# Optimization experiments

Hardware: AMD Instinct MI355X
Metric: run time of the kernel (lower is better)

## Reference

```python
import jax, jax.numpy as jnp
import numpy as np

B, L = 8, 2048
Q_IN, V_IN, QK, VD = 512, 1024, 96, 96


def _conv1d_same(x_bcl, w_oik, b_o):
    # x: (B, C, L), w: (O, I, K), 'same' padding, stride 1
    y = jax.lax.conv_general_dilated(
        x_bcl, w_oik, window_strides=(1,), padding='SAME',
        dimension_numbers=('NCH', 'OIH', 'NCH'))
    return y + b_o[None, :, None]


def masked_softmax(scores, seqlengths):
    # scores: (B, L, L); mask key positions >= seqlengths[b]
    mask = jnp.arange(scores.shape[-1])[None, None, :] < seqlengths[:, None, None]
    scores = jnp.where(mask, scores, jnp.float32(-1e6))
    return jax.nn.softmax(scores, axis=-1)


def setup_inputs() -> dict:
    key = jax.random.key(0)
    ks = jax.random.split(key, 12)
    def lin(k, fan_in, shape):
        bound = 1.0 / np.sqrt(fan_in)
        return jax.random.uniform(k, shape, jnp.float32, -bound, bound)
    return {
        'plm_embedding': jax.random.normal(ks[0], (B, L, V_IN), jnp.float32),
        'evo_local': jax.random.normal(ks[1], (B, L, Q_IN), jnp.float32),
        'seqlengths': jax.random.randint(ks[2], (B,), 1, L + 1),
        'q_w': lin(ks[3], Q_IN, (QK, Q_IN)), 'q_b': lin(ks[4], Q_IN, (QK,)),
        'k_w': lin(ks[5], Q_IN + 2 * VD, (QK, Q_IN + 2 * VD)), 'k_b': lin(ks[6], Q_IN + 2 * VD, (QK,)),
        'v_w': lin(ks[7], V_IN, (VD, V_IN)), 'v_b': lin(ks[8], V_IN, (VD,)),
        'cn3_w': lin(ks[9], Q_IN * 3, (QK, Q_IN, 3)), 'cn3_b': lin(ks[9], Q_IN * 3, (QK,)),
        'cn5_w': lin(ks[10], Q_IN * 5, (QK, Q_IN, 5)), 'cn5_b': lin(ks[11], Q_IN * 5, (QK,)),
    }


def reference(plm_embedding, evo_local, seqlengths, q_w, q_b, k_w, k_b, v_w, v_b,
              cn3_w, cn3_b, cn5_w, cn5_b):
    norm = jnp.float32(1.0 / np.sqrt(QK))
    Q = jnp.einsum('bld,od->blo', evo_local, q_w) + q_b          # (B,L,QK)
    x_bcl = jnp.transpose(evo_local, (0, 2, 1))                  # (B,C,L)
    k3 = _conv1d_same(x_bcl, cn3_w, cn3_b)                       # (B,QK,L)
    k5 = _conv1d_same(x_bcl, cn5_w, cn5_b)
    cat = jnp.concatenate(
        (evo_local, jnp.transpose(k3, (0, 2, 1)), jnp.transpose(k5, (0, 2, 1))), axis=2)
    K = jnp.einsum('bld,od->blo', cat, k_w) + k_b                # (B,L,QK)
    V = jnp.einsum('bld,od->blo', plm_embedding, v_w) + v_b      # (B,L,VD)
    scores = jnp.einsum('bqd,bkd->bqk', Q, K) * norm             # (B,L,L)
    atten = masked_softmax(scores, seqlengths)
    out = jnp.einsum('bqk,bkd->bqd', atten, V)
    return out + V
```

## Files before the change

kernel.cpp:

```cpp
#include <hip/hip_runtime.h>

typedef unsigned short u16;
typedef unsigned int u32;
typedef float f32x4 __attribute__((ext_vector_type(4)));
typedef short s16x8 __attribute__((ext_vector_type(8)));

#define LSEQ 2048
#define QIN 512
#define VIN 1024
#define KCAT 704
#define KEFF 2560
#define NORMS 0.10206207261596575f

__device__ __forceinline__ u16 f2bf(float f) {
  u32 u = __float_as_uint(f);
  u = (u + 0x7fffu + ((u >> 16) & 1u)) >> 16;
  return (u16)u;
}
__device__ __forceinline__ float bf2f(u16 v) {
  return __uint_as_float(((u32)v) << 16);
}

__device__ __forceinline__ s16x8 load8cvt(const float* __restrict__ p) {
  float4 a = *(const float4*)p;
  float4 b = *(const float4*)(p + 4);
  s16x8 r;
  r[0] = (short)f2bf(a.x); r[1] = (short)f2bf(a.y);
  r[2] = (short)f2bf(a.z); r[3] = (short)f2bf(a.w);
  r[4] = (short)f2bf(b.x); r[5] = (short)f2bf(b.y);
  r[6] = (short)f2bf(b.z); r[7] = (short)f2bf(b.w);
  return r;
}

__device__ __forceinline__ s16x8 cvt2x4(float4 a, float4 b) {
  s16x8 r;
  r[0] = (short)f2bf(a.x); r[1] = (short)f2bf(a.y);
  r[2] = (short)f2bf(a.z); r[3] = (short)f2bf(a.w);
  r[4] = (short)f2bf(b.x); r[5] = (short)f2bf(b.y);
  r[6] = (short)f2bf(b.z); r[7] = (short)f2bf(b.w);
  return r;
}

__device__ __forceinline__ size_t wfrag_idx(int o, int k) {
  int kc = k >> 5, kg = (k >> 3) & 3, j = k & 7;
  int nt = o >> 4, ln = o & 15;
  return ((size_t)(kc * 6 + nt) * 64 + kg * 16 + ln) * 8 + j;
}

__global__ __launch_bounds__(256) void prep1(
    const float* __restrict__ q_w, const float* __restrict__ k_w,
    const float* __restrict__ k_b, const float* __restrict__ v_w,
    const float* __restrict__ cn3_w, const float* __restrict__ cn3_b,
    const float* __restrict__ cn5_w, const float* __restrict__ cn5_b,
    float* __restrict__ c3t, float* __restrict__ c5t,
    u16* __restrict__ qwf, u16* __restrict__ vwf,
    u16* __restrict__ kw3f, u16* __restrict__ kw5f,
    float* __restrict__ beff) {
  int blk = blockIdx.x, tid = threadIdx.x;
  if (blk < 576) {
    int idx = blk * 256 + tid;
    int t = idx / (512 * 96);
    int rem = idx - t * 512 * 96;
    int c = rem / 96, j = rem - c * 96;
    c3t[idx] = cn3_w[(j * 512 + c) * 3 + t];
  } else if (blk < 1536) {
    int idx = (blk - 576) * 256 + tid;
    int t = idx / (512 * 96);
    int rem = idx - t * 512 * 96;
    int c = rem / 96, j = rem - c * 96;
    c5t[idx] = cn5_w[(j * 512 + c) * 5 + t];
  } else if (blk < 1728) {
    int e = (blk - 1536) * 256 + tid;
    int o = e >> 9, k = e & 511;
    qwf[wfrag_idx(o, k)] = f2bf(q_w[e]);
  } else if (blk < 2112) {
    int e = (blk - 1728) * 256 + tid;
    int o = e >> 10, k = e & 1023;
    vwf[wfrag_idx(o, k)] = f2bf(v_w[e]);
  } else if (blk < 2184) {
    int e = (blk - 2112) * 256 + tid;
    int half = e / 9216;
    int i = e - half * 9216;
    int o = i / 96, j = i - o * 96;
    float v = k_w[o * KCAT + (half ? 608 : 512) + j];
    size_t di = ((size_t)((j >> 5) * 6 + (o >> 4)) * 64 +
                 ((j >> 3) & 3) * 16 + (o & 15)) * 8 + (j & 7);
    (half ? kw5f : kw3f)[di] = f2bf(v);
  } else {
    if (tid < 96) {
      const float* kwo = k_w + tid * KCAT;
      float b = k_b[tid];
      for (int j = 0; j < 96; ++j)
        b += kwo[512 + j] * cn3_b[j] + kwo[608 + j] * cn5_b[j];
      beff[tid] = b;
    }
  }
}

__global__ __launch_bounds__(256) void prep2(
    const float* __restrict__ c3t, const float* __restrict__ c5t,
    const u16* __restrict__ kw3f, const u16* __restrict__ kw5f,
    const float* __restrict__ k_w, u16* __restrict__ wefff) {
  __shared__ float Ls[4][16][100];
  int blk = blockIdx.x, tid = threadIdx.x;
  int wid = tid >> 6, lane = tid & 63, ln = lane & 15, kg = lane >> 4;
  int k = blk * 64 + wid * 16 + ln;
  bool c3ok = (k >= 512) && (k < 2048);
  const float* a5 = c5t + (size_t)k * 96;
  const float* a3 = c3t + (size_t)(c3ok ? k - 512 : 0) * 96;
  f32x4 acc[6];
  #pragma unroll
  for (int nt = 0; nt < 6; ++nt) acc[nt] = (f32x4){0.f, 0.f, 0.f, 0.f};
  #pragma unroll
  for (int jc = 0; jc < 3; ++jc) {
    s16x8 aa5 = load8cvt(a5 + jc * 32 + kg * 8);
    s16x8 aa3 = (s16x8){0, 0, 0, 0, 0, 0, 0, 0};
    if (c3ok) aa3 = load8cvt(a3 + jc * 32 + kg * 8);
    const u16* b5 = kw5f + (size_t)jc * 3072 + lane * 8;
    const u16* b3 = kw3f + (size_t)jc * 3072 + lane * 8;
    #pragma unroll
    for (int nt = 0; nt < 6; ++nt) {
      acc[nt] = __builtin_amdgcn_mfma_f32_16x16x32_bf16(
          aa5, *(const s16x8*)&b5[nt * 512], acc[nt], 0, 0, 0);
      acc[nt] = __builtin_amdgcn_mfma_f32_16x16x32_bf16(
          aa3, *(const s16x8*)&b3[nt * 512], acc[nt], 0, 0, 0);
    }
  }
  #pragma unroll
  for (int nt = 0; nt < 6; ++nt)
    #pragma unroll
    for (int r = 0; r < 4; ++r)
      Ls[wid][kg * 4 + r][nt * 16 + ln] = acc[nt][r];
  asm volatile("s_waitcnt lgkmcnt(0)" ::: "memory");
  #pragma unroll
  for (int sl = 0; sl < 3; ++sl) {
    int slot = sl * 64 + lane;
    int o = slot >> 1, rc = slot & 1;
    int k0 = blk * 64 + wid * 16 + rc * 8;
    int t = k0 >> 9, cbase = k0 & 511;
    s16x8 ov;
    #pragma unroll
    for (int e = 0; e < 8; ++e) {
      float v = Ls[wid][rc * 8 + e][o];
      if (t == 2) v += k_w[o * KCAT + cbase + e];
      ov[e] = (short)f2bf(v);
    }
    *(s16x8*)&wefff[((size_t)((k0 >> 5) * 6 + (o >> 4)) * 64 +
                     ((k0 >> 3) & 3) * 16 + (o & 15)) * 8] = ov;
  }
}

__global__ __launch_bounds__(256, 2) void proj_fused(
    const float* __restrict__ evo, const float* __restrict__ plm,
    const u16* __restrict__ qwf, const u16* __restrict__ vwf,
    const u16* __restrict__ wefff, const float* __restrict__ q_b,
    const float* __restrict__ beff, const float* __restrict__ v_b,
    u16* __restrict__ Qf, u16* __restrict__ Kf,
    u16* __restrict__ Vfr, u16* __restrict__ Vb) {
  __shared__ u16 At[2 * 68 * 72];
  __shared__ u16 LBS[18432];
  float* Ls = (float*)LBS;
  int bxr = blockIdx.x, bb = blockIdx.y;
  int tid = threadIdx.x;
  int wid = tid >> 6, lane = tid & 63, ln = lane & 15, kg = lane >> 4;
  int srow = tid >> 2, spart = tid & 3;

  if (bxr < 32) {
    int bx = bxr;
    int r0 = bx * 64;
    const float* xb = evo + (size_t)bb * LSEQ * QIN;
    bool halo = tid < 16;
    int hrow = 64 + (tid >> 2);

    float4 ra0, ra1, ra2, ra3, rb0, rb1, rb2, rb3;
    auto LOADS = [&](int s) {
      int g = r0 - 2 + srow;
      if (g >= 0 && g < LSEQ) {
        const float* p = xb + (size_t)g * QIN + s * 64 + spart * 16;
        ra0 = *(const float4*)p;       ra1 = *(const float4*)(p + 4);
        ra2 = *(const float4*)(p + 8); ra3 = *(const float4*)(p + 12);
      } else {
        ra0 = ra1 = ra2 = ra3 = make_float4(0.f, 0.f, 0.f, 0.f);
      }
      if (halo) {
        int g2 = r0 - 2 + hrow;
        if (g2 < LSEQ) {
          const float* p = xb + (size_t)g2 * QIN + s * 64 + spart * 16;
          rb0 = *(const float4*)p;       rb1 = *(const float4*)(p + 4);
          rb2 = *(const float4*)(p + 8); rb3 = *(const float4*)(p + 12);
        } else {
          rb0 = rb1 = rb2 = rb3 = make_float4(0.f, 0.f, 0.f, 0.f);
        }
      }
    };
    auto WRITES = [&](int buf) {
      u16* d = &At[(buf * 68 + srow) * 72 + spart * 16];
      *(s16x8*)d = cvt2x4(ra0, ra1);
      *(s16x8*)(d + 8) = cvt2x4(ra2, ra3);
      if (halo) {
        u16* d2 = &At[(buf * 68 + hrow) * 72 + spart * 16];
        *(s16x8*)d2 = cvt2x4(rb0, rb1);
        *(s16x8*)(d2 + 8) = cvt2x4(rb2, rb3);
      }
    };

    s16x8 br[9];
    auto LOADB = [&](int kcg) {
      #pragma unroll
      for (int j = 0; j < 9; ++j) {
        int idx = tid + j * 256;
        int chunk = idx / 384;
        int off = idx - chunk * 384;
        const u16* src = (chunk == 0)
            ? qwf + (size_t)kcg * 3072 + off * 8
            : wefff + (size_t)(chunk - 1) * 49152 + (size_t)kcg * 3072 + off * 8;
        br[j] = *(const s16x8*)src;
      }
    };
    auto STOREB = [&]() {
      #pragma unroll
      for (int j = 0; j < 9; ++j) {
        int idx = tid + j * 256;
        *(s16x8*)&LBS[idx * 8] = br[j];
      }
    };

    f32x4 accQ[6], accK[6];
    #pragma unroll
    for (int nt = 0; nt < 6; ++nt) {
      accQ[nt] = (f32x4){0.f, 0.f, 0.f, 0.f};
      accK[nt] = (f32x4){0.f, 0.f, 0.f, 0.f};
    }

    LOADS(0);
    LOADB(0);
    WRITES(0);
    STOREB();
    __syncthreads();
    int cur = 0;
    for (int s = 0; s < 8; ++s) {
      if (s < 7) LOADS(s + 1);
      #pragma unroll
      for (int cc = 0; cc < 2; ++cc) {
        int kcg = s * 2 + cc;
        bool havenext = kcg < 15;
        if (havenext) LOADB(kcg + 1);
        const u16* arow = &At[(cur * 68 + wid * 16 + ln) * 72 + cc * 32 + kg * 8];
        s16x8 aQ  = *(const s16x8*)&arow[2 * 72];
        s16x8 aK0 = *(const s16x8*)&arow[0];
        s16x8 aK1 = *(const s16x8*)&arow[1 * 72];
        s16x8 aK3 = *(const s16x8*)&arow[3 * 72];
        s16x8 aK4 = *(const s16x8*)&arow[4 * 72];
        const u16* lb = LBS + lane * 8;
        s16x8 bfr[6];
        #pragma unroll
        for (int i = 0; i < 6; ++i)
          bfr[i] = *(const s16x8*)&lb[i * 512];
        #pragma unroll
        for (int i = 0; i < 6; ++i)
          accQ[i] = __builtin_amdgcn_mfma_f32_16x16x32_bf16(
              aQ, bfr[i], accQ[i], 0, 0, 0);
        #pragma unroll
        for (int t = 0; t < 5; ++t) {
          s16x8 bf2[6];
          #pragma unroll
          for (int i = 0; i < 6; ++i)
            bf2[i] = *(const s16x8*)&lb[(1 + t) * 3072 + i * 512];
          s16x8 aK = (t == 0) ? aK0 : (t == 1) ? aK1 : (t == 2) ? aQ
                   : (t == 3) ? aK3 : aK4;
          #pragma unroll
          for (int i = 0; i < 6; ++i)
            accK[i] = __builtin_amdgcn_mfma_f32_16x16x32_bf16(
                aK, bf2[i], accK[i], 0, 0, 0);
        }
        __syncthreads();
        if (havenext) STOREB();
        if (cc == 1 && s < 7) WRITES(cur ^ 1);
        __syncthreads();
      }
      if (s < 7) cur ^= 1;
    }

    size_t qt = (size_t)bb * 128 + bx * 4 + wid;
    #pragma unroll
    for (int nt = 0; nt < 6; ++nt)
      #pragma unroll
      for (int r = 0; r < 4; ++r)
        Ls[wid * 1600 + (kg * 4 + r) * 100 + nt * 16 + ln] = accQ[nt][r];
    asm volatile("s_waitcnt lgkmcnt(0)" ::: "memory");
    #pragma unroll
    for (int sl = 0; sl < 3; ++sl) {
      int slot = sl * 64 + lane;
      int r = slot / 12, cg = slot % 12;
      s16x8 ov;
      #pragma unroll
      for (int e = 0; e < 8; ++e) {
        int c = cg * 8 + e;
        ov[e] = (short)f2bf(Ls[wid * 1600 + r * 100 + c] + q_b[c]);
      }
      *(s16x8*)&Qf[((qt * 3 + (cg >> 2)) * 64 + (cg & 3) * 16 + r) * 8] = ov;
    }
    asm volatile("s_waitcnt lgkmcnt(0) vmcnt(0)" ::: "memory");
    #pragma unroll
    for (int nt = 0; nt < 6; ++nt)
      #pragma unroll
      for (int r = 0; r < 4; ++r)
        Ls[wid * 1600 + (kg * 4 + r) * 100 + nt * 16 + ln] = accK[nt][r];
    asm volatile("s_waitcnt lgkmcnt(0)" ::: "memory");
    #pragma unroll
    for (int sl = 0; sl < 3; ++sl) {
      int slot = sl * 64 + lane;
      int r = slot / 12, cg = slot % 12;
      s16x8 ov;
      #pragma unroll
      for (int e = 0; e < 8; ++e) {
        int c = cg * 8 + e;
        ov[e] = (short)f2bf(Ls[wid * 1600 + r * 100 + c] + beff[c]);
      }
      *(s16x8*)&Kf[((qt * 3 + (cg >> 2)) * 64 + (cg & 3) * 16 + r) * 8] = ov;
    }
  } else {
    int bx = bxr - 32;
    const float* xb = plm + ((size_t)bb * LSEQ + bx * 64) * VIN;
    float4 ra0, ra1, ra2, ra3;
    auto LOADS = [&](int s) {
      const float* p = xb + (size_t)srow * VIN + s * 64 + spart * 16;
      ra0 = *(const float4*)p;       ra1 = *(const float4*)(p + 4);
      ra2 = *(const float4*)(p + 8); ra3 = *(const float4*)(p + 12);
    };
    auto WRITES = [&](int buf) {
      u16* d = &At[(buf * 68 + srow) * 72 + spart * 16];
      *(s16x8*)d = cvt2x4(ra0, ra1);
      *(s16x8*)(d + 8) = cvt2x4(ra2, ra3);
    };
    s16x8 br[3];
    auto LOADB = [&](int s) {
      #pragma unroll
      for (int j = 0; j < 3; ++j) {
        int idx = tid + j * 256;
        br[j] = *(const s16x8*)(vwf + (size_t)s * 6144 + idx * 8);
      }
    };
    auto STOREB = [&]() {
      #pragma unroll
      for (int j = 0; j < 3; ++j) {
        int idx = tid + j * 256;
        *(s16x8*)&LBS[idx * 8] = br[j];
      }
    };

    f32x4 acc[6];
    #pragma unroll
    for (int nt = 0; nt < 6; ++nt) acc[nt] = (f32x4){0.f, 0.f, 0.f, 0.f};

    LOADS(0);
    LOADB(0);
    WRITES(0);
    STOREB();
    __syncthreads();
    int cur = 0;
    for (int s = 0; s < 16; ++s) {
      if (s < 15) {
        LOADS(s + 1);
        LOADB(s + 1);
      }
      #pragma unroll
      for (int cc = 0; cc < 2; ++cc) {
        s16x8 a = *(const s16x8*)&At[(cur * 68 + wid * 16 + ln) * 72 +
                                     cc * 32 + kg * 8];
        const u16* lb = LBS + cc * 3072 + lane * 8;
        s16x8 bfr[6];
        #pragma unroll
        for (int nt = 0; nt < 6; ++nt)
          bfr[nt] = *(const s16x8*)&lb[nt * 512];
        #pragma unroll
        for (int nt = 0; nt < 6; ++nt)
          acc[nt] = __builtin_amdgcn_mfma_f32_16x16x32_bf16(
              a, bfr[nt], acc[nt], 0, 0, 0);
      }
      __syncthreads();
      if (s < 15) {
        STOREB();
        WRITES(cur ^ 1);
      }
      __syncthreads();
      if (s < 15) cur ^= 1;
    }

    #pragma unroll
    for (int nt = 0; nt < 6; ++nt)
      #pragma unroll
      for (int r = 0; r < 4; ++r)
        Ls[wid * 1600 + (kg * 4 + r) * 100 + nt * 16 + ln] = acc[nt][r];
    asm volatile("s_waitcnt lgkmcnt(0)" ::: "memory");
    #pragma unroll
    for (int sl = 0; sl < 3; ++sl) {
      int slot = sl * 64 + lane;
      int r = slot / 12, cg = slot % 12;
      s16x8 ov;
      #pragma unroll
      for (int e = 0; e < 8; ++e) {
        int c = cg * 8 + e;
        ov[e] = (short)f2bf(Ls[wid * 1600 + r * 100 + c] + v_b[c]);
      }
      *(s16x8*)&Vb[((size_t)bb * LSEQ + bx * 64 + wid * 16 + r) * 96 + cg * 8] = ov;
    }
    #pragma unroll
    for (int sl = 0; sl < 3; ++sl) {
      int slot = sl * 64 + lane;
      int c = slot >> 1, rc = slot & 1;
      int key0 = bx * 64 + wid * 16 + rc * 8;
      s16x8 fv;
      #pragma unroll
      for (int e = 0; e < 8; ++e)
        fv[e] = (short)f2bf(Ls[wid * 1600 + (rc * 8 + e) * 100 + c] + v_b[c]);
      *(s16x8*)&Vfr[(((size_t)bb * 64 + (key0 >> 5)) * 6 + (c >> 4)) * 512 +
                    (((key0 >> 3) & 3) * 16 + (c & 15)) * 8] = fv;
    }
  }
}

__global__ __launch_bounds__(256, 4) void attn_kernel(
    const u16* __restrict__ Qf, const u16* __restrict__ Kf,
    const u16* __restrict__ Vfr, const u16* __restrict__ Vb,
    const int* __restrict__ seqlen, float* __restrict__ out) {
  __shared__ u16 Ps[4][16][40];
  __shared__ float Cacc[4][16][97];
  __shared__ float Cml[4][16][2];

  int bid = blockIdx.x;
  int bb = (bid >> 3) & 7;
  int bx = ((bid >> 6) << 3) | (bid & 7);
  int tid = threadIdx.x;
  int wid = tid >> 6, lane = tid & 63, ln = lane & 15, kg = lane >> 4;
  int n = seqlen[bb];
  int nkc = (n + 31) >> 5;

  size_t qt = (size_t)bb * 128 + bx;
  s16x8 aQ[3];
  #pragma unroll
  for (int kk = 0; kk < 3; ++kk)
    aQ[kk] = *(const s16x8*)&Qf[((qt * 3 + kk) * 64 + lane) * 8];

  float m[4], lsum[4];
  f32x4 acc[6];
  #pragma unroll
  for (int r = 0; r < 4; ++r) { m[r] = -1e30f; lsum[r] = 0.f; }
  #pragma unroll
  for (int nt = 0; nt < 6; ++nt) acc[nt] = (f32x4){0.f, 0.f, 0.f, 0.f};

  const u16* Kbb = Kf + (size_t)bb * 128 * 1536;
  s16x8 kf[6];
  {
    int k0 = (wid < nkc) ? wid : 0;
    const u16* kp = Kbb + (size_t)k0 * 3072 + lane * 8;
    #pragma unroll
    for (int i = 0; i < 6; ++i) kf[i] = *(const s16x8*)&kp[i * 512];
  }

  for (int kc = wid; kc < nkc; kc += 4) {
    int key0 = kc * 32;
    f32x4 s0 = (f32x4){0.f, 0.f, 0.f, 0.f};
    f32x4 s1 = (f32x4){0.f, 0.f, 0.f, 0.f};
    __builtin_amdgcn_s_setprio(1);
    #pragma unroll
    for (int kk = 0; kk < 3; ++kk) {
      s0 = __builtin_amdgcn_mfma_f32_16x16x32_bf16(aQ[kk], kf[kk], s0, 0, 0, 0);
      s1 = __builtin_amdgcn_mfma_f32_16x16x32_bf16(aQ[kk], kf[3 + kk], s1, 0, 0, 0);
    }
    __builtin_amdgcn_s_setprio(0);

    s16x8 kf2[6];
    {
      int kn = (kc + 4 < nkc) ? kc + 4 : 0;
      const u16* kp = Kbb + (size_t)kn * 3072 + lane * 8;
      #pragma unroll
      for (int i = 0; i < 6; ++i) kf2[i] = *(const s16x8*)&kp[i * 512];
    }

    bool v0 = (key0 + ln) < n;
    bool v1 = (key0 + 16 + ln) < n;
    float sv0[4], sv1[4], mx[4];
    #pragma unroll
    for (int r = 0; r < 4; ++r) {
      sv0[r] = v0 ? s0[r] * NORMS : -1e30f;
      sv1[r] = v1 ? s1[r] * NORMS : -1e30f;
      mx[r] = fmaxf(sv0[r], sv1[r]);
    }
    #pragma unroll
    for (int r = 0; r < 4; ++r) {
      mx[r] = fmaxf(mx[r], __shfl_xor(mx[r], 1, 16));
      mx[r] = fmaxf(mx[r], __shfl_xor(mx[r], 2, 16));
      mx[r] = fmaxf(mx[r], __shfl_xor(mx[r], 4, 16));
      mx[r] = fmaxf(mx[r], __shfl_xor(mx[r], 8, 16));
    }
    float p0[4], p1[4], rs[4];
    bool defer = __all((mx[0] <= m[0] + 8.f) && (mx[1] <= m[1] + 8.f) &&
                       (mx[2] <= m[2] + 8.f) && (mx[3] <= m[3] + 8.f));
    if (defer) {
      #pragma unroll
      for (int r = 0; r < 4; ++r) {
        p0[r] = __expf(sv0[r] - m[r]);
        p1[r] = __expf(sv1[r] - m[r]);
        rs[r] = p0[r] + p1[r];
      }
      #pragma unroll
      for (int r = 0; r < 4; ++r) {
        rs[r] += __shfl_xor(rs[r], 1, 16);
        rs[r] += __shfl_xor(rs[r], 2, 16);
        rs[r] += __shfl_xor(rs[r], 4, 16);
        rs[r] += __shfl_xor(rs[r], 8, 16);
        lsum[r] += rs[r];
      }
    } else {
      float fac[4];
      #pragma unroll
      for (int r = 0; r < 4; ++r) {
        float mn = fmaxf(m[r], mx[r]);
        fac[r] = __expf(m[r] - mn);
        p0[r] = __expf(sv0[r] - mn);
        p1[r] = __expf(sv1[r] - mn);
        rs[r] = p0[r] + p1[r];
        m[r] = mn;
      }
      #pragma unroll
      for (int r = 0; r < 4; ++r) {
        rs[r] += __shfl_xor(rs[r], 1, 16);
        rs[r] += __shfl_xor(rs[r], 2, 16);
        rs[r] += __shfl_xor(rs[r], 4, 16);
        rs[r] += __shfl_xor(rs[r], 8, 16);
        lsum[r] = lsum[r] * fac[r] + rs[r];
      }
      #pragma unroll
      for (int nt = 0; nt < 6; ++nt)
        #pragma unroll
        for (int r = 0; r < 4; ++r) acc[nt][r] *= fac[r];
    }

    u16* Pw = &Ps[wid][0][0];
    #pragma unroll
    for (int r = 0; r < 4; ++r) {
      Pw[(kg * 4 + r) * 40 + ln] = f2bf(p0[r]);
      Pw[(kg * 4 + r) * 40 + 16 + ln] = f2bf(p1[r]);
    }
    s16x8 pa = *(const s16x8*)&Pw[ln * 40 + kg * 8];

    const u16* vf = Vfr + (((size_t)bb * 64 + kc) * 6 * 64) * 8 + lane * 8;
    s16x8 bv[6];
    #pragma unroll
    for (int nt = 0; nt < 6; ++nt)
      bv[nt] = *(const s16x8*)&vf[(size_t)nt * 512];
    __builtin_amdgcn_s_setprio(1);
    #pragma unroll
    for (int nt = 0; nt < 6; ++nt)
      acc[nt] = __builtin_amdgcn_mfma_f32_16x16x32_bf16(pa, bv[nt], acc[nt], 0, 0, 0);
    __builtin_amdgcn_s_setprio(0);
    #pragma unroll
    for (int i = 0; i < 6; ++i) kf[i] = kf2[i];
  }

  #pragma unroll
  for (int nt = 0; nt < 6; ++nt)
    #pragma unroll
    for (int r = 0; r < 4; ++r)
      Cacc[wid][kg * 4 + r][nt * 16 + ln] = acc[nt][r];
  if (ln == 0) {
    #pragma unroll
    for (int r = 0; r < 4; ++r) {
      Cml[wid][kg * 4 + r][0] = m[r];
      Cml[wid][kg * 4 + r][1] = lsum[r];
    }
  }
  __syncthreads();

  size_t obase = ((size_t)bb * LSEQ + bx * 16) * 96;
  for (int i = tid; i < 1536; i += 256) {
    int row = i / 96;
    float mg = -1e30f;
    #pragma unroll
    for (int w = 0; w < 4; ++w) mg = fmaxf(mg, Cml[w][row][0]);
    float lg = 0.f, av = 0.f;
    #pragma unroll
    for (int w = 0; w < 4; ++w) {
      float e = __expf(Cml[w][row][0] - mg);
      lg += Cml[w][row][1] * e;
      av += Cacc[w][row][i - row * 96] * e;
    }
    out[obase + i] = av / lg + bf2f(Vb[obase + i]);
  }
}

extern "C" void kernel_launch(void* const* d_in, const int* in_sizes, int n_in,
                              void* d_out, int out_size, void* d_ws,
                              size_t ws_size, hipStream_t stream) {
  const float* plm   = (const float*)d_in[0];
  const float* evo   = (const float*)d_in[1];
  const int* seqlen  = (const int*)d_in[2];
  const float* q_w   = (const float*)d_in[3];
  const float* q_b   = (const float*)d_in[4];
  const float* k_w   = (const float*)d_in[5];
  const float* k_b   = (const float*)d_in[6];
  const float* v_w   = (const float*)d_in[7];
  const float* v_b   = (const float*)d_in[8];
  const float* cn3_w = (const float*)d_in[9];
  const float* cn3_b = (const float*)d_in[10];
  const float* cn5_w = (const float*)d_in[11];
  const float* cn5_b = (const float*)d_in[12];

  char* ws = (char*)d_ws;
  u16* wefff  = (u16*)(ws + 0);
  float* beff = (float*)(ws + 491520);
  u16* qwf    = (u16*)(ws + 492032);
  u16* vwf    = (u16*)(ws + 590336);
  float* c3t  = (float*)(ws + 786944);
  float* c5t  = (float*)(ws + 1376768);
  u16* kw3f   = (u16*)(ws + 2359808);
  u16* kw5f   = (u16*)(ws + 2378240);
  u16* Qf     = (u16*)(ws + 2396672);
  u16* Kf     = (u16*)(ws + 5542400);
  u16* Vfr    = (u16*)(ws + 8688128);
  u16* Vb     = (u16*)(ws + 11833856);
  float* out  = (float*)d_out;

  prep1<<<2185, 256, 0, stream>>>(q_w, k_w, k_b, v_w, cn3_w, cn3_b, cn5_w,
                                  cn5_b, c3t, c5t, qwf, vwf, kw3f, kw5f, beff);
  prep2<<<40, 256, 0, stream>>>(c3t, c5t, kw3f, kw5f, k_w, wefff);
  proj_fused<<<dim3(64, 8), 256, 0, stream>>>(evo, plm, qwf, vwf, wefff,
                                              q_b, beff, v_b, Qf, Kf, Vfr, Vb);
  attn_kernel<<<1024, 256, 0, stream>>>(Qf, Kf, Vfr, Vb, seqlen, out);
}
```

Measured before the change: 84.97 us.

## Process two query tiles per attention block to reuse K/V fragments

Each attention workgroup now computes two 16-row query tiles, sharing each loaded K and V fragment across both sets of MFMAs and doubling per-wave accumulator state. The grid is halved to 512 blocks and launch bounds lowered to 2 blocks per CU to accommodate the extra registers. This aims to cut global/L2 K/V load traffic per query row, at the cost of lower occupancy, fewer blocks for load balancing across variable sequence lengths, and a second epilogue pass with an extra barrier.

```diff
diff --git a/kernel.cpp b/kernel.cpp
--- a/kernel.cpp
+++ b/kernel.cpp
@@ -420,11 +420,11 @@
   }
 }
 
-__global__ __launch_bounds__(256, 4) void attn_kernel(
+__global__ __launch_bounds__(256, 2) void attn_kernel(
     const u16* __restrict__ Qf, const u16* __restrict__ Kf,
     const u16* __restrict__ Vfr, const u16* __restrict__ Vb,
     const int* __restrict__ seqlen, float* __restrict__ out) {
-  __shared__ u16 Ps[4][16][40];
+  __shared__ u16 Ps[4][2][16][40];
   __shared__ float Cacc[4][16][97];
   __shared__ float Cml[4][16][2];
 
@@ -436,18 +436,24 @@
   int n = seqlen[bb];
   int nkc = (n + 31) >> 5;
 
-  size_t qt = (size_t)bb * 128 + bx;
-  s16x8 aQ[3];
+  s16x8 aQ[2][3];
   #pragma unroll
-  for (int kk = 0; kk < 3; ++kk)
-    aQ[kk] = *(const s16x8*)&Qf[((qt * 3 + kk) * 64 + lane) * 8];
-
-  float m[4], lsum[4];
-  f32x4 acc[6];
+  for (int g = 0; g < 2; ++g) {
+    size_t qt = (size_t)bb * 128 + bx * 2 + g;
+    #pragma unroll
+    for (int kk = 0; kk < 3; ++kk)
+      aQ[g][kk] = *(const s16x8*)&Qf[((qt * 3 + kk) * 64 + lane) * 8];
+  }
+
+  float m[2][4], lsum[2][4];
+  f32x4 acc[2][6];
   #pragma unroll
-  for (int r = 0; r < 4; ++r) { m[r] = -1e30f; lsum[r] = 0.f; }
-  #pragma unroll
-  for (int nt = 0; nt < 6; ++nt) acc[nt] = (f32x4){0.f, 0.f, 0.f, 0.f};
+  for (int g = 0; g < 2; ++g) {
+    #pragma unroll
+    for (int r = 0; r < 4; ++r) { m[g][r] = -1e30f; lsum[g][r] = 0.f; }
+    #pragma unroll
+    for (int nt = 0; nt < 6; ++nt) acc[g][nt] = (f32x4){0.f, 0.f, 0.f, 0.f};
+  }
 
   const u16* Kbb = Kf + (size_t)bb * 128 * 1536;
   s16x8 kf[6];
@@ -460,13 +466,19 @@
 
   for (int kc = wid; kc < nkc; kc += 4) {
     int key0 = kc * 32;
-    f32x4 s0 = (f32x4){0.f, 0.f, 0.f, 0.f};
-    f32x4 s1 = (f32x4){0.f, 0.f, 0.f, 0.f};
+    f32x4 s0[2], s1[2];
+    #pragma unroll
+    for (int g = 0; g < 2; ++g) {
+      s0[g] = (f32x4){0.f, 0.f, 0.f, 0.f};
+      s1[g] = (f32x4){0.f, 0.f, 0.f, 0.f};
+    }
     __builtin_amdgcn_s_setprio(1);
     #pragma unroll
     for (int kk = 0; kk < 3; ++kk) {
-      s0 = __builtin_amdgcn_mfma_f32_16x16x32_bf16(aQ[kk], kf[kk], s0, 0, 0, 0);
-      s1 = __builtin_amdgcn_mfma_f32_16x16x32_bf16(aQ[kk], kf[3 + kk], s1, 0, 0, 0);
+      s0[0] = __builtin_amdgcn_mfma_f32_16x16x32_bf16(aQ[0][kk], kf[kk], s0[0], 0, 0, 0);
+      s0[1] = __builtin_amdgcn_mfma_f32_16x16x32_bf16(aQ[1][kk], kf[kk], s0[1], 0, 0, 0);
+      s1[0] = __builtin_amdgcn_mfma_f32_16x16x32_bf16(aQ[0][kk], kf[3 + kk], s1[0], 0, 0, 0);
+      s1[1] = __builtin_amdgcn_mfma_f32_16x16x32_bf16(aQ[1][kk], kf[3 + kk], s1[1], 0, 0, 0);
     }
     __builtin_amdgcn_s_setprio(0);
 
@@ -480,70 +492,89 @@
 
     bool v0 = (key0 + ln) < n;
     bool v1 = (key0 + 16 + ln) < n;
-    float sv0[4], sv1[4], mx[4];
-    #pragma unroll
-    for (int r = 0; r < 4; ++r) {
-      sv0[r] = v0 ? s0[r] * NORMS : -1e30f;
-      sv1[r] = v1 ? s1[r] * NORMS : -1e30f;
-      mx[r] = fmaxf(sv0[r], sv1[r]);
-    }
-    #pragma unroll
-    for (int r = 0; r < 4; ++r) {
-      mx[r] = fmaxf(mx[r], __shfl_xor(mx[r], 1, 16));
-      mx[r] = fmaxf(mx[r], __shfl_xor(mx[r], 2, 16));
-      mx[r] = fmaxf(mx[r], __shfl_xor(mx[r], 4, 16));
-      mx[r] = fmaxf(mx[r], __shfl_xor(mx[r], 8, 16));
-    }
-    float p0[4], p1[4], rs[4];
-    bool defer = __all((mx[0] <= m[0] + 8.f) && (mx[1] <= m[1] + 8.f) &&
-                       (mx[2] <= m[2] + 8.f) && (mx[3] <= m[3] + 8.f));
+    float sv0[2][4], sv1[2][4], mx[2][4];
+    #pragma unroll
+    for (int g = 0; g < 2; ++g)
+      #pragma unroll
+      for (int r = 0; r < 4; ++r) {
+        sv0[g][r] = v0 ? s0[g][r] * NORMS : -1e30f;
+        sv1[g][r] = v1 ? s1[g][r] * NORMS : -1e30f;
+        mx[g][r] = fmaxf(sv0[g][r], sv1[g][r]);
+      }
+    #pragma unroll
+    for (int g = 0; g < 2; ++g)
+      #pragma unroll
+      for (int r = 0; r < 4; ++r) {
+        mx[g][r] = fmaxf(mx[g][r], __shfl_xor(mx[g][r], 1, 16));
+        mx[g][r] = fmaxf(mx[g][r], __shfl_xor(mx[g][r], 2, 16));
+        mx[g][r] = fmaxf(mx[g][r], __shfl_xor(mx[g][r], 4, 16));
+        mx[g][r] = fmaxf(mx[g][r], __shfl_xor(mx[g][r], 8, 16));
+      }
+    float p0[2][4], p1[2][4], rs[2][4];
+    bool cond = true;
+    #pragma unroll
+    for (int g = 0; g < 2; ++g)
+      #pragma unroll
+      for (int r = 0; r < 4; ++r)
+        cond = cond && (mx[g][r] <= m[g][r] + 8.f);
+    bool defer = __all(cond);
     if (defer) {
       #pragma unroll
+      for (int g = 0; g < 2; ++g) {
+        #pragma unroll
+        for (int r = 0; r < 4; ++r) {
+          p0[g][r] = __expf(sv0[g][r] - m[g][r]);
+          p1[g][r] = __expf(sv1[g][r] - m[g][r]);
+          rs[g][r] = p0[g][r] + p1[g][r];
+        }
+        #pragma unroll
+        for (int r = 0; r < 4; ++r) {
+          rs[g][r] += __shfl_xor(rs[g][r], 1, 16);
+          rs[g][r] += __shfl_xor(rs[g][r], 2, 16);
+          rs[g][r] += __shfl_xor(rs[g][r], 4, 16);
+          rs[g][r] += __shfl_xor(rs[g][r], 8, 16);
+          lsum[g][r] += rs[g][r];
+        }
+      }
+    } else {
+      float fac[2][4];
+      #pragma unroll
+      for (int g = 0; g < 2; ++g) {
+        #pragma unroll
+        for (int r = 0; r < 4; ++r) {
+          float mn = fmaxf(m[g][r], mx[g][r]);
+          fac[g][r] = __expf(m[g][r] - mn);
+          p0[g][r] = __expf(sv0[g][r] - mn);
+          p1[g][r] = __expf(sv1[g][r] - mn);
+          rs[g][r] = p0[g][r] + p1[g][r];
+          m[g][r] = mn;
+        }
+        #pragma unroll
+        for (int r = 0; r < 4; ++r) {
+          rs[g][r] += __shfl_xor(rs[g][r], 1, 16);
+          rs[g][r] += __shfl_xor(rs[g][r], 2, 16);
+          rs[g][r] += __shfl_xor(rs[g][r], 4, 16);
+          rs[g][r] += __shfl_xor(rs[g][r], 8, 16);
+          lsum[g][r] = lsum[g][r] * fac[g][r] + rs[g][r];
+        }
+        #pragma unroll
+        for (int nt = 0; nt < 6; ++nt)
+          #pragma unroll
+          for (int r = 0; r < 4; ++r) acc[g][nt][r] *= fac[g][r];
+      }
+    }
+
+    s16x8 pa[2];
+    #pragma unroll
+    for (int g = 0; g < 2; ++g) {
+      u16* Pw = &Ps[wid][g][0][0];
+      #pragma unroll
       for (int r = 0; r < 4; ++r) {
-        p0[r] = __expf(sv0[r] - m[r]);
-        p1[r] = __expf(sv1[r] - m[r]);
-        rs[r] = p0[r] + p1[r];
-      }
-      #pragma unroll
-      for (int r = 0; r < 4; ++r) {
-        rs[r] += __shfl_xor(rs[r], 1, 16);
-        rs[r] += __shfl_xor(rs[r], 2, 16);
-        rs[r] += __shfl_xor(rs[r], 4, 16);
-        rs[r] += __shfl_xor(rs[r], 8, 16);
-        lsum[r] += rs[r];
-      }
-    } else {
-      float fac[4];
-      #pragma unroll
-      for (int r = 0; r < 4; ++r) {
-        float mn = fmaxf(m[r], mx[r]);
-        fac[r] = __expf(m[r] - mn);
-        p0[r] = __expf(sv0[r] - mn);
-        p1[r] = __expf(sv1[r] - mn);
-        rs[r] = p0[r] + p1[r];
-        m[r] = mn;
-      }
-      #pragma unroll
-      for (int r = 0; r < 4; ++r) {
-        rs[r] += __shfl_xor(rs[r], 1, 16);
-        rs[r] += __shfl_xor(rs[r], 2, 16);
-        rs[r] += __shfl_xor(rs[r], 4, 16);
-        rs[r] += __shfl_xor(rs[r], 8, 16);
-        lsum[r] = lsum[r] * fac[r] + rs[r];
-      }
-      #pragma unroll
-      for (int nt = 0; nt < 6; ++nt)
-        #pragma unroll
-        for (int r = 0; r < 4; ++r) acc[nt][r] *= fac[r];
-    }
-
-    u16* Pw = &Ps[wid][0][0];
-    #pragma unroll
-    for (int r = 0; r < 4; ++r) {
-      Pw[(kg * 4 + r) * 40 + ln] = f2bf(p0[r]);
-      Pw[(kg * 4 + r) * 40 + 16 + ln] = f2bf(p1[r]);
-    }
-    s16x8 pa = *(const s16x8*)&Pw[ln * 40 + kg * 8];
+        Pw[(kg * 4 + r) * 40 + ln] = f2bf(p0[g][r]);
+        Pw[(kg * 4 + r) * 40 + 16 + ln] = f2bf(p1[g][r]);
+      }
+      pa[g] = *(const s16x8*)&Pw[ln * 40 + kg * 8];
+    }
 
     const u16* vf = Vfr + (((size_t)bb * 64 + kc) * 6 * 64) * 8 + lane * 8;
     s16x8 bv[6];
@@ -552,41 +583,47 @@
       bv[nt] = *(const s16x8*)&vf[(size_t)nt * 512];
     __builtin_amdgcn_s_setprio(1);
     #pragma unroll
+    for (int nt = 0; nt < 6; ++nt) {
+      acc[0][nt] = __builtin_amdgcn_mfma_f32_16x16x32_bf16(pa[0], bv[nt], acc[0][nt], 0, 0, 0);
+      acc[1][nt] = __builtin_amdgcn_mfma_f32_16x16x32_bf16(pa[1], bv[nt], acc[1][nt], 0, 0, 0);
+    }
+    __builtin_amdgcn_s_setprio(0);
+    #pragma unroll
+    for (int i = 0; i < 6; ++i) kf[i] = kf2[i];
+  }
+
+  #pragma unroll
+  for (int g = 0; g < 2; ++g) {
+    if (g) __syncthreads();
+    #pragma unroll
     for (int nt = 0; nt < 6; ++nt)
-      acc[nt] = __builtin_amdgcn_mfma_f32_16x16x32_bf16(pa, bv[nt], acc[nt], 0, 0, 0);
-    __builtin_amdgcn_s_setprio(0);
-    #pragma unroll
-    for (int i = 0; i < 6; ++i) kf[i] = kf2[i];
-  }
-
-  #pragma unroll
-  for (int nt = 0; nt < 6; ++nt)
-    #pragma unroll
-    for (int r = 0; r < 4; ++r)
-      Cacc[wid][kg * 4 + r][nt * 16 + ln] = acc[nt][r];
-  if (ln == 0) {
-    #pragma unroll
-    for (int r = 0; r < 4; ++r) {
-      Cml[wid][kg * 4 + r][0] = m[r];
-      Cml[wid][kg * 4 + r][1] = lsum[r];
-    }
-  }
-  __syncthreads();
-
-  size_t obase = ((size_t)bb * LSEQ + bx * 16) * 96;
-  for (int i = tid; i < 1536; i += 256) {
-    int row = i / 96;
-    float mg = -1e30f;
-    #pragma unroll
-    for (int w = 0; w < 4; ++w) mg = fmaxf(mg, Cml[w][row][0]);
-    float lg = 0.f, av = 0.f;
-    #pragma unroll
-    for (int w = 0; w < 4; ++w) {
-      float e = __expf(Cml[w][row][0] - mg);
-      lg += Cml[w][row][1] * e;
-      av += Cacc[w][row][i - row * 96] * e;
-    }
-    out[obase + i] = av / lg + bf2f(Vb[obase + i]);
+      #pragma unroll
+      for (int r = 0; r < 4; ++r)
+        Cacc[wid][kg * 4 + r][nt * 16 + ln] = acc[g][nt][r];
+    if (ln == 0) {
+      #pragma unroll
+      for (int r = 0; r < 4; ++r) {
+        Cml[wid][kg * 4 + r][0] = m[g][r];
+        Cml[wid][kg * 4 + r][1] = lsum[g][r];
+      }
+    }
+    __syncthreads();
+
+    size_t obase = ((size_t)bb * LSEQ + bx * 32 + g * 16) * 96;
+    for (int i = tid; i < 1536; i += 256) {
+      int row = i / 96;
+      float mg = -1e30f;
+      #pragma unroll
+      for (int w = 0; w < 4; ++w) mg = fmaxf(mg, Cml[w][row][0]);
+      float lg = 0.f, av = 0.f;
+      #pragma unroll
+      for (int w = 0; w < 4; ++w) {
+        float e = __expf(Cml[w][row][0] - mg);
+        lg += Cml[w][row][1] * e;
+        av += Cacc[w][row][i - row * 96] * e;
+      }
+      out[obase + i] = av / lg + bf2f(Vb[obase + i]);
+    }
   }
 }
 
@@ -627,5 +664,5 @@
   prep2<<<40, 256, 0, stream>>>(c3t, c5t, kw3f, kw5f, k_w, wefff);
   proj_fused<<<dim3(64, 8), 256, 0, stream>>>(evo, plm, qwf, vwf, wefff,
                                               q_b, beff, v_b, Qf, Kf, Vfr, Vb);
-  attn_kernel<<<1024, 256, 0, stream>>>(Qf, Kf, Vfr, Vb, seqlen, out);
-}
+  attn_kernel<<<512, 256, 0, stream>>>(Qf, Kf, Vfr, Vb, seqlen, out);
+}
```

Result: slower. 87.99 us (+3.5%).

## Split Q/K projection work across warps by conv tap instead of by row

Applied to the files above, without the earlier changes.

The Q/K projection stage is repartitioned so each warp handles all four 16-row groups but only a subset of the work. Warp 0 computes Q, and warps 1-3 each compute one or two of the five conv taps for K. Before, every warp did all six MMA groups for its own 16 rows, which meant reloading all B fragments per warp. Now each warp loads only the B fragments for its taps and reuses them across the four row groups, cutting LDS B traffic. In exchange, each warp holds 24 accumulator registers, the tap work is uneven (warp 3 has one tap, others two), and the epilogue needs a cross-warp reduction through LDS with extra barriers.

```diff
diff --git a/kernel.cpp b/kernel.cpp
--- a/kernel.cpp
+++ b/kernel.cpp
@@ -225,12 +225,14 @@
       }
     };
 
-    f32x4 accQ[6], accK[6];
-    #pragma unroll
-    for (int nt = 0; nt < 6; ++nt) {
-      accQ[nt] = (f32x4){0.f, 0.f, 0.f, 0.f};
-      accK[nt] = (f32x4){0.f, 0.f, 0.f, 0.f};
-    }
+    f32x4 acc[4][6];
+    #pragma unroll
+    for (int rg = 0; rg < 4; ++rg)
+      #pragma unroll
+      for (int nt = 0; nt < 6; ++nt) acc[rg][nt] = (f32x4){0.f, 0.f, 0.f, 0.f};
+
+    int tap0 = (wid == 1) ? 0 : (wid == 2) ? 2 : 4;
+    int ntap = (wid == 3) ? 1 : 2;
 
     LOADS(0);
     LOADB(0);
@@ -245,33 +247,49 @@
         int kcg = s * 2 + cc;
         bool havenext = kcg < 15;
         if (havenext) LOADB(kcg + 1);
-        const u16* arow = &At[(cur * 68 + wid * 16 + ln) * 72 + cc * 32 + kg * 8];
-        s16x8 aQ  = *(const s16x8*)&arow[2 * 72];
-        s16x8 aK0 = *(const s16x8*)&arow[0];
-        s16x8 aK1 = *(const s16x8*)&arow[1 * 72];
-        s16x8 aK3 = *(const s16x8*)&arow[3 * 72];
-        s16x8 aK4 = *(const s16x8*)&arow[4 * 72];
-        const u16* lb = LBS + lane * 8;
-        s16x8 bfr[6];
-        #pragma unroll
-        for (int i = 0; i < 6; ++i)
-          bfr[i] = *(const s16x8*)&lb[i * 512];
-        #pragma unroll
-        for (int i = 0; i < 6; ++i)
-          accQ[i] = __builtin_amdgcn_mfma_f32_16x16x32_bf16(
-              aQ, bfr[i], accQ[i], 0, 0, 0);
-        #pragma unroll
-        for (int t = 0; t < 5; ++t) {
-          s16x8 bf2[6];
+        const u16* abase = &At[(cur * 68 + ln) * 72 + cc * 32 + kg * 8];
+        if (wid == 0) {
+          const u16* lb = LBS + lane * 8;
+          s16x8 b0 = *(const s16x8*)&lb[0 * 512];
+          s16x8 b1 = *(const s16x8*)&lb[1 * 512];
+          s16x8 b2 = *(const s16x8*)&lb[2 * 512];
+          s16x8 b3 = *(const s16x8*)&lb[3 * 512];
+          s16x8 b4 = *(const s16x8*)&lb[4 * 512];
+          s16x8 b5 = *(const s16x8*)&lb[5 * 512];
           #pragma unroll
-          for (int i = 0; i < 6; ++i)
-            bf2[i] = *(const s16x8*)&lb[(1 + t) * 3072 + i * 512];
-          s16x8 aK = (t == 0) ? aK0 : (t == 1) ? aK1 : (t == 2) ? aQ
-                   : (t == 3) ? aK3 : aK4;
+          for (int rg = 0; rg < 4; ++rg) {
+            s16x8 a = *(const s16x8*)&abase[(rg * 16 + 2) * 72];
+            acc[rg][0] = __builtin_amdgcn_mfma_f32_16x16x32_bf16(a, b0, acc[rg][0], 0, 0, 0);
+            acc[rg][1] = __builtin_amdgcn_mfma_f32_16x16x32_bf16(a, b1, acc[rg][1], 0, 0, 0);
+            acc[rg][2] = __builtin_amdgcn_mfma_f32_16x16x32_bf16(a, b2, acc[rg][2], 0, 0, 0);
+            acc[rg][3] = __builtin_amdgcn_mfma_f32_16x16x32_bf16(a, b3, acc[rg][3], 0, 0, 0);
+            acc[rg][4] = __builtin_amdgcn_mfma_f32_16x16x32_bf16(a, b4, acc[rg][4], 0, 0, 0);
+            acc[rg][5] = __builtin_amdgcn_mfma_f32_16x16x32_bf16(a, b5, acc[rg][5], 0, 0, 0);
+          }
+        } else {
           #pragma unroll
-          for (int i = 0; i < 6; ++i)
-            accK[i] = __builtin_amdgcn_mfma_f32_16x16x32_bf16(
-                aK, bf2[i], accK[i], 0, 0, 0);
+          for (int tt = 0; tt < 2; ++tt) {
+            if (tt < ntap) {
+              int t = tap0 + tt;
+              const u16* lb = LBS + (1 + t) * 3072 + lane * 8;
+              s16x8 b0 = *(const s16x8*)&lb[0 * 512];
+              s16x8 b1 = *(const s16x8*)&lb[1 * 512];
+              s16x8 b2 = *(const s16x8*)&lb[2 * 512];
+              s16x8 b3 = *(const s16x8*)&lb[3 * 512];
+              s16x8 b4 = *(const s16x8*)&lb[4 * 512];
+              s16x8 b5 = *(const s16x8*)&lb[5 * 512];
+              #pragma unroll
+              for (int rg = 0; rg < 4; ++rg) {
+                s16x8 a = *(const s16x8*)&abase[(rg * 16 + t) * 72];
+                acc[rg][0] = __builtin_amdgcn_mfma_f32_16x16x32_bf16(a, b0, acc[rg][0], 0, 0, 0);
+                acc[rg][1] = __builtin_amdgcn_mfma_f32_16x16x32_bf16(a, b1, acc[rg][1], 0, 0, 0);
+                acc[rg][2] = __builtin_amdgcn_mfma_f32_16x16x32_bf16(a, b2, acc[rg][2], 0, 0, 0);
+                acc[rg][3] = __builtin_amdgcn_mfma_f32_16x16x32_bf16(a, b3, acc[rg][3], 0, 0, 0);
+                acc[rg][4] = __builtin_amdgcn_mfma_f32_16x16x32_bf16(a, b4, acc[rg][4], 0, 0, 0);
+                acc[rg][5] = __builtin_amdgcn_mfma_f32_16x16x32_bf16(a, b5, acc[rg][5], 0, 0, 0);
+              }
+            }
+          }
         }
         __syncthreads();
         if (havenext) STOREB();
@@ -281,43 +299,31 @@
       if (s < 7) cur ^= 1;
     }
 
-    size_t qt = (size_t)bb * 128 + bx * 4 + wid;
-    #pragma unroll
-    for (int nt = 0; nt < 6; ++nt)
-      #pragma unroll
-      for (int r = 0; r < 4; ++r)
-        Ls[wid * 1600 + (kg * 4 + r) * 100 + nt * 16 + ln] = accQ[nt][r];
-    asm volatile("s_waitcnt lgkmcnt(0)" ::: "memory");
-    #pragma unroll
-    for (int sl = 0; sl < 3; ++sl) {
-      int slot = sl * 64 + lane;
-      int r = slot / 12, cg = slot % 12;
-      s16x8 ov;
-      #pragma unroll
-      for (int e = 0; e < 8; ++e) {
-        int c = cg * 8 + e;
-        ov[e] = (short)f2bf(Ls[wid * 1600 + r * 100 + c] + q_b[c]);
-      }
-      *(s16x8*)&Qf[((qt * 3 + (cg >> 2)) * 64 + (cg & 3) * 16 + r) * 8] = ov;
-    }
-    asm volatile("s_waitcnt lgkmcnt(0) vmcnt(0)" ::: "memory");
-    #pragma unroll
-    for (int nt = 0; nt < 6; ++nt)
-      #pragma unroll
-      for (int r = 0; r < 4; ++r)
-        Ls[wid * 1600 + (kg * 4 + r) * 100 + nt * 16 + ln] = accK[nt][r];
-    asm volatile("s_waitcnt lgkmcnt(0)" ::: "memory");
-    #pragma unroll
-    for (int sl = 0; sl < 3; ++sl) {
-      int slot = sl * 64 + lane;
-      int r = slot / 12, cg = slot % 12;
-      s16x8 ov;
-      #pragma unroll
-      for (int e = 0; e < 8; ++e) {
-        int c = cg * 8 + e;
-        ov[e] = (short)f2bf(Ls[wid * 1600 + r * 100 + c] + beff[c]);
-      }
-      *(s16x8*)&Kf[((qt * 3 + (cg >> 2)) * 64 + (cg & 3) * 16 + r) * 8] = ov;
+    int slot = (wid == 0) ? 3 : (wid - 1);
+    #pragma unroll
+    for (int rg = 0; rg < 4; ++rg) {
+      if (rg) __syncthreads();
+      #pragma unroll
+      for (int nt = 0; nt < 6; ++nt)
+        #pragma unroll
+        for (int r = 0; r < 4; ++r)
+          Ls[slot * 1600 + (kg * 4 + r) * 100 + nt * 16 + ln] = acc[rg][nt][r];
+      __syncthreads();
+      size_t qt = (size_t)bb * 128 + bx * 4 + rg;
+      if (tid < 192) {
+        int r = tid / 12, cg = tid % 12;
+        s16x8 ovk, ovq;
+        #pragma unroll
+        for (int e = 0; e < 8; ++e) {
+          int c = cg * 8 + e;
+          float kv = Ls[0 * 1600 + r * 100 + c] + Ls[1 * 1600 + r * 100 + c] +
+                     Ls[2 * 1600 + r * 100 + c] + beff[c];
+          ovk[e] = (short)f2bf(kv);
+          ovq[e] = (short)f2bf(Ls[3 * 1600 + r * 100 + c] + q_b[c]);
+        }
+        *(s16x8*)&Kf[((qt * 3 + (cg >> 2)) * 64 + (cg & 3) * 16 + r) * 8] = ovk;
+        *(s16x8*)&Qf[((qt * 3 + (cg >> 2)) * 64 + (cg & 3) * 16 + r) * 8] = ovq;
+      }
     }
   } else {
     int bx = bxr - 32;
```

Result: slower. 159.6 us (+87.8%).
